# Kernel optimization log

Measured on AMD Instinct MI355X. Metric: run time of the kernel, lower is better.

Reference implementation:

```python
import jax, jax.numpy as jnp
import numpy as np

# FCHL19 representation (Christensen et al., JCP 2020), as implemented by
# QMLightning's pairlist_gpu/egto_gpu/fchl_gpu CUDA kernels, re-expressed as
# dense masked pair/triplet tensors (non-periodic: cell/inv_cell empty).
SPECIES = np.array([1.0, 6.0, 7.0, 8.0], dtype=np.float32)
NSPEC = 4
NRS2 = 24
NRS3 = 20
RCUT = 8.0
ETA2 = 0.32
ETA3 = 2.7
TWO_BODY_DECAY = 1.8
THREE_BODY_DECAY = 0.57
THREE_BODY_WEIGHT = float(np.sqrt(ETA3 / np.pi) * 13.4)  # module pre-scales weight
RS2 = np.linspace(0.0, RCUT, NRS2 + 1)[1:].astype(np.float32)
RS3 = np.linspace(0.0, RCUT, NRS3 + 1)[1:].astype(np.float32)
NPAIR = NSPEC * (NSPEC + 1) // 2  # unordered species pairs -> 10

def _pair_map():
    M = np.zeros((NSPEC, NSPEC, NPAIR), np.float32)
    i = 0
    for p in range(NSPEC):
        for q in range(p, NSPEC):
            M[p, q, i] = 1.0
            M[q, p, i] = 1.0
            i += 1
    return M
PAIR_MAP = _pair_map()

B_MOL, MAX_ATOMS = 64, 28


def setup_inputs() -> dict:
    key = jax.random.key(0)
    k1, k2, k3 = jax.random.split(key, 3)
    X = jax.random.uniform(k1, (B_MOL, MAX_ATOMS, 3), jnp.float32) * 6.0
    atom_counts = jax.random.randint(k2, (B_MOL,), 24, MAX_ATOMS + 1).astype(jnp.int32)
    zidx = jax.random.randint(k3, (B_MOL, MAX_ATOMS), 0, NSPEC)
    valid = jnp.arange(MAX_ATOMS)[None, :] < atom_counts[:, None]
    Z = jnp.where(valid, jnp.asarray(SPECIES)[zidx], 0.0).astype(jnp.float32)
    atomIDs = jnp.arange(B_MOL * MAX_ATOMS, dtype=jnp.int32)
    molIDs = jnp.repeat(jnp.arange(B_MOL, dtype=jnp.int32), MAX_ATOMS)
    return {"X": X, "Z": Z, "atomIDs": atomIDs, "molIDs": molIDs, "atom_counts": atom_counts}


def _fchl(X, Z, atom_counts):
    B, N, _ = X.shape
    valid = jnp.arange(N)[None, :] < atom_counts[:, None]               # [B,N]
    diff = X[:, :, None, :] - X[:, None, :, :]                          # [B,N,N,3]
    d2 = jnp.sum(diff * diff, -1)
    eye = jnp.eye(N, dtype=bool)[None]
    pair_ok = valid[:, :, None] & valid[:, None, :] & (~eye)
    r = jnp.sqrt(jnp.where(pair_ok, d2, 1.0))                           # grad-safe distances
    within = pair_ok & (r < RCUT)
    fc = jnp.where(within, 0.5 * (jnp.cos(jnp.pi * r / RCUT) + 1.0), 0.0)
    oh = (Z[:, :, None] == jnp.asarray(SPECIES)[None, None, :]).astype(X.dtype)  # [B,N,S]

    # --- two-body: log-normal radial expansion, 1/r^decay scaling, cosine cutoff ---
    ln = jnp.log1p(ETA2 / (r * r))                                      # sigma^2
    mu = jnp.log(r) - 0.5 * ln
    rs2 = jnp.asarray(RS2)
    norm = 1.0 / (jnp.sqrt(ln)[..., None] * np.float32(np.sqrt(2.0 * np.pi)) * rs2)
    radial2 = (fc / jnp.power(r, TWO_BODY_DECAY))[..., None] * norm * \
        jnp.exp(-(jnp.log(rs2) - mu[..., None]) ** 2 / (2.0 * ln[..., None]))     # [B,N,N,M]
    rep2 = jnp.einsum('bijm,bjs->bism', radial2, oh).reshape(B, N, NSPEC * NRS2)

    # --- three-body: Axilrod-Teller-weighted radial x Fourier(order 1) angular ---
    rij = r[:, :, :, None]   # [B,i,j,1] -> broadcast over k
    rik = r[:, :, None, :]
    rjk = r[:, None, :, :]
    triu = (jnp.arange(N)[:, None] < jnp.arange(N)[None, :])[None, None]  # j<k
    m3 = within[:, :, :, None] & within[:, :, None, :] & triu
    rjk_s = jnp.where(m3, rjk, 1.0)
    cos_i = jnp.where(m3, (rij**2 + rik**2 - rjk_s**2) / (2.0 * rij * rik), 0.0)
    cos_j = (rij**2 + rjk_s**2 - rik**2) / (2.0 * rij * rjk_s)
    cos_k = (rik**2 + rjk_s**2 - rij**2) / (2.0 * rik * rjk_s)
    atm = (1.0 + 3.0 * cos_i * cos_j * cos_k) / jnp.power(rij * rik * rjk_s, THREE_BODY_DECAY)
    w = jnp.where(m3, THREE_BODY_WEIGHT * atm * fc[:, :, :, None] * fc[:, :, None, :], 0.0)
    c = jnp.clip(cos_i, -1.0, 1.0)
    s = jnp.sqrt(jnp.clip(1.0 - c * c, 1e-12, 1.0))
    ang = jnp.stack([2.0 * c, 2.0 * s], -1) * w[..., None]              # [B,N,N,N,2]
    radial3 = jnp.exp(-ETA3 * (0.5 * (rij + rik)[..., None] - jnp.asarray(RS3)) ** 2)  # [B,N,N,N,L]
    pair_oh = jnp.einsum('bjp,bkq,pqP->bjkP', oh, oh, jnp.asarray(PAIR_MAP))           # [B,N,N,10]
    t = jnp.einsum('bijka,bjkP->bijkaP', ang, pair_oh)
    rep3 = jnp.einsum('bijkaP,bijkl->biPla', t, radial3).reshape(B, N, NPAIR * NRS3 * 2)

    return jnp.concatenate([rep2, rep3], -1)  # [B,N,496]


def reference(X, Z, atomIDs, molIDs, atom_counts):
    # atomIDs/molIDs are CUDA block-assignment bookkeeping; math doesn't use them.
    return _fchl(X, Z, atom_counts)
```

## Files before the change

kernel.cpp:

```cpp
#include <hip/hip_runtime.h>

#define B_MOL 64
#define MAXN 28
#define NSPEC 4
#define NRS2 24
#define NRS3 20
#define NPAIR 10
#define NCOMB 378
#define REP2_LEN (NSPEC * NRS2)
#define REP3_LEN (NPAIR * NRS3 * 2)
#define OUT_LEN (REP2_LEN + REP3_LEN)
#define RCUT 8.0f
#define ETA2 0.32f
#define ETA3 2.7f
#define LOG2E 1.4426950408889634f
#define LN2F 0.6931471805599453f
#define W3 12.4225783348083f

__device__ __forceinline__ float hexp2(float x) { return __builtin_amdgcn_exp2f(x); }
__device__ __forceinline__ float hlog2(float x) { return __builtin_amdgcn_logf(x); }
__device__ __forceinline__ float hrcp(float x)  { return __builtin_amdgcn_rcpf(x); }
__device__ __forceinline__ float hrsq(float x)  { return __builtin_amdgcn_rsqf(x); }
__device__ __forceinline__ float hcos_rev(float t) { return __builtin_amdgcn_cosf(t); }

__device__ __forceinline__ void decode_pair(int idx, int& j, int& k) {
    int jj = (int)((55.0f - sqrtf(3025.0f - 8.0f * (float)idx)) * 0.5f);
    while (27 * (jj + 1) - ((jj + 1) * jj) / 2 <= idx) ++jj;
    while (27 * jj - (jj * (jj - 1)) / 2 > idx) --jj;
    int off = 27 * jj - (jj * (jj - 1)) / 2;
    j = jj;
    k = jj + 1 + (idx - off);
}

__global__ __launch_bounds__(256) void fchl_kernel(
    const float* __restrict__ X,
    const float* __restrict__ Z,
    const int* __restrict__ counts,
    float* __restrict__ out)
{
    const int i = blockIdx.x;
    const int b = blockIdx.y;
    const int tid = threadIdx.x;
    const int cnt = counts[b];

    __shared__ float sx[MAXN], sy[MAXN], szc[MAXN];
    __shared__ int   sspec[MAXN];
    __shared__ int   s_win[MAXN];
    __shared__ float s_r[MAXN], s_fc[MAXN], s_mu[MAXN], s_i2ln[MAXN], s_pref[MAXN];
    __shared__ int   cntP[NPAIR], curP[NPAIR], baseP[NPAIR];
    __shared__ float4 s_pair[NCOMB];

    if (tid < MAXN) {
        sx[tid]  = X[(b * MAXN + tid) * 3 + 0];
        sy[tid]  = X[(b * MAXN + tid) * 3 + 1];
        szc[tid] = X[(b * MAXN + tid) * 3 + 2];
        float z = Z[b * MAXN + tid];
        int s = -1;
        if (z == 1.0f) s = 0;
        else if (z == 6.0f) s = 1;
        else if (z == 7.0f) s = 2;
        else if (z == 8.0f) s = 3;
        sspec[tid] = s;
    }
    if (tid < NPAIR) cntP[tid] = 0;
    __syncthreads();

    const bool valid_i = (i < cnt);

    if (tid < MAXN) {
        const int j = tid;
        float dx = sx[i] - sx[j], dy = sy[i] - sy[j], dz = szc[i] - szc[j];
        float r = sqrtf(dx * dx + dy * dy + dz * dz);
        bool w = valid_i && (j < cnt) && (j != i) && (r < RCUT);
        s_win[j] = w ? 1 : 0;
        if (w) {
            float fc = 0.5f * (hcos_rev(r * (1.0f / 16.0f)) + 1.0f);
            float ln = LN2F * hlog2(1.0f + ETA2 * hrcp(r * r));
            float lr = LN2F * hlog2(r);
            s_r[j] = r;
            s_fc[j] = fc;
            s_mu[j] = lr - 0.5f * ln;
            s_i2ln[j] = LOG2E / (2.0f * ln);
            s_pref[j] = fc * hexp2(-1.8f * hlog2(r)) * hrsq(ln);
        } else {
            s_r[j] = 1.0f; s_fc[j] = 0.0f; s_mu[j] = 0.0f;
            s_i2ln[j] = 1.0f; s_pref[j] = 0.0f;
        }
    }
    __syncthreads();

    for (int idx = tid; idx < NCOMB; idx += 256) {
        int j, k; decode_pair(idx, j, k);
        if (s_win[j] && s_win[k]) {
            int pj = sspec[j], pk = sspec[k];
            int p = min(pj, pk), q = max(pj, pk);
            int P = p * NSPEC - (p * (p - 1)) / 2 + (q - p);
            atomicAdd(&cntP[P], 1);
        }
    }
    __syncthreads();
    if (tid == 0) {
        int acc = 0;
        #pragma unroll
        for (int p = 0; p < NPAIR; ++p) {
            baseP[p] = acc; curP[p] = acc; acc += cntP[p];
        }
    }
    __syncthreads();

    for (int idx = tid; idx < NCOMB; idx += 256) {
        int j, k; decode_pair(idx, j, k);
        if (!(s_win[j] && s_win[k])) continue;

        float rij = s_r[j], rik = s_r[k];
        float dx = sx[j] - sx[k], dy = sy[j] - sy[k], dz = szc[j] - szc[k];
        float rjk = sqrtf(dx * dx + dy * dy + dz * dz);

        float rij2 = rij * rij, rik2 = rik * rik, rjk2 = rjk * rjk;
        float cos_i = (rij2 + rik2 - rjk2) * 0.5f * hrcp(rij * rik);
        float cos_j = (rij2 + rjk2 - rik2) * 0.5f * hrcp(rij * rjk);
        float cos_k = (rik2 + rjk2 - rij2) * 0.5f * hrcp(rik * rjk);

        float atm = (1.0f + 3.0f * cos_i * cos_j * cos_k)
                    * hexp2(-0.57f * hlog2(rij * rik * rjk));
        float w = W3 * atm * s_fc[j] * s_fc[k];

        float c = fminf(fmaxf(cos_i, -1.0f), 1.0f);
        float sn = sqrtf(fminf(fmaxf(1.0f - c * c, 1e-12f), 1.0f));

        int pj = sspec[j], pk = sspec[k];
        int p = min(pj, pk), q = max(pj, pk);
        int P = p * NSPEC - (p * (p - 1)) / 2 + (q - p);

        int slot = atomicAdd(&curP[P], 1);
        s_pair[slot] = make_float4(0.5f * (rij + rik), 2.0f * c * w, 2.0f * sn * w, 0.0f);
    }
    __syncthreads();

    float* orow = out + (size_t)(b * MAXN + i) * OUT_LEN;

    if (tid < NPAIR * NRS3) {
        const int P = tid / NRS3;
        const int l = tid % NRS3;
        const float rs = 0.4f * (float)(l + 1);
        float acc0 = 0.0f, acc1 = 0.0f;
        const int s0 = baseP[P], s1 = s0 + cntP[P];
        for (int s = s0; s < s1; ++s) {
            float4 pd = s_pair[s];
            float dd = pd.x - rs;
            float e = hexp2(-(ETA3 * LOG2E) * dd * dd);
            acc0 += pd.y * e;
            acc1 += pd.z * e;
        }
        orow[REP2_LEN + P * (NRS3 * 2) + l * 2 + 0] = acc0;
        orow[REP2_LEN + P * (NRS3 * 2) + l * 2 + 1] = acc1;
    }

    if (tid >= 160) {
        const int t2 = tid - 160;
        const int sp = t2 / NRS2;
        const int m = t2 % NRS2;
        const float rs2 = (float)(m + 1) * (8.0f / 24.0f);
        const float lrs2 = LN2F * hlog2(rs2);
        const float nrm = 0.3989422804014327f / rs2;
        float acc = 0.0f;
        #pragma unroll
        for (int j = 0; j < MAXN; ++j) {
            if (s_win[j] && sspec[j] == sp) {
                float d = lrs2 - s_mu[j];
                acc += s_pref[j] * hexp2(-d * d * s_i2ln[j]);
            }
        }
        orow[sp * NRS2 + m] = acc * nrm;
    }
}

extern "C" void kernel_launch(void* const* d_in, const int* in_sizes, int n_in,
                              void* d_out, int out_size, void* d_ws, size_t ws_size,
                              hipStream_t stream) {
    const float* X = (const float*)d_in[0];
    const float* Z = (const float*)d_in[1];
    const int* counts = (const int*)d_in[4];
    float* out = (float*)d_out;

    dim3 grid(MAXN, B_MOL);
    dim3 block(256);
    hipLaunchKernelGGL(fchl_kernel, grid, block, 0, stream, X, Z, counts, out);
}
```

Baseline: 20.69 us.

## Restructure FCHL kernel phases to cut barriers and overlap two-body work

Replaces the arithmetic pair decode with a constant-memory lookup table. Merges coordinate loading with the pair-distance stage, which removes one barrier. The thread-0 prefix scan is replaced by per-thread prefix sums over the pair counts, removing another barrier. The two-body radial computation moves onto otherwise idle threads during the counting phase, and pair tags are cached in shared memory so the species pair index is not recomputed. In exchange each thread does some redundant prefix-sum work and adds a constant-memory load.

New measurement: 24.17 us. 1.17x slower.

```diff
diff --git a/kernel.cpp b/kernel.cpp
--- a/kernel.cpp
+++ b/kernel.cpp
@@ -23,14 +23,16 @@
 __device__ __forceinline__ float hrsq(float x)  { return __builtin_amdgcn_rsqf(x); }
 __device__ __forceinline__ float hcos_rev(float t) { return __builtin_amdgcn_cosf(t); }
 
-__device__ __forceinline__ void decode_pair(int idx, int& j, int& k) {
-    int jj = (int)((55.0f - sqrtf(3025.0f - 8.0f * (float)idx)) * 0.5f);
-    while (27 * (jj + 1) - ((jj + 1) * jj) / 2 <= idx) ++jj;
-    while (27 * jj - (jj * (jj - 1)) / 2 > idx) --jj;
-    int off = 27 * jj - (jj * (jj - 1)) / 2;
-    j = jj;
-    k = jj + 1 + (idx - off);
+struct PairTab { unsigned short jk[NCOMB]; };
+static constexpr PairTab make_tab() {
+    PairTab t{};
+    int idx = 0;
+    for (int j = 0; j < MAXN; ++j)
+        for (int k = j + 1; k < MAXN; ++k)
+            t.jk[idx++] = (unsigned short)((j << 8) | k);
+    return t;
 }
+__constant__ PairTab PT = make_tab();
 
 __global__ __launch_bounds__(256) void fchl_kernel(
     const float* __restrict__ X,
@@ -47,31 +49,32 @@
     __shared__ int   sspec[MAXN];
     __shared__ int   s_win[MAXN];
     __shared__ float s_r[MAXN], s_fc[MAXN], s_mu[MAXN], s_i2ln[MAXN], s_pref[MAXN];
-    __shared__ int   cntP[NPAIR], curP[NPAIR], baseP[NPAIR];
+    __shared__ int   cntP[NPAIR], curP[NPAIR];
+    __shared__ signed char s_ptag[NCOMB];
     __shared__ float4 s_pair[NCOMB];
 
+    float* orow = out + (size_t)(b * MAXN + i) * OUT_LEN;
+
     if (tid < MAXN) {
-        sx[tid]  = X[(b * MAXN + tid) * 3 + 0];
-        sy[tid]  = X[(b * MAXN + tid) * 3 + 1];
-        szc[tid] = X[(b * MAXN + tid) * 3 + 2];
-        float z = Z[b * MAXN + tid];
+        const int j = tid;
+        float xj = X[(b * MAXN + j) * 3 + 0];
+        float yj = X[(b * MAXN + j) * 3 + 1];
+        float zj = X[(b * MAXN + j) * 3 + 2];
+        sx[j] = xj; sy[j] = yj; szc[j] = zj;
+        float z = Z[b * MAXN + j];
         int s = -1;
         if (z == 1.0f) s = 0;
         else if (z == 6.0f) s = 1;
         else if (z == 7.0f) s = 2;
         else if (z == 8.0f) s = 3;
-        sspec[tid] = s;
-    }
-    if (tid < NPAIR) cntP[tid] = 0;
-    __syncthreads();
+        sspec[j] = s;
 
-    const bool valid_i = (i < cnt);
-
-    if (tid < MAXN) {
-        const int j = tid;
-        float dx = sx[i] - sx[j], dy = sy[i] - sy[j], dz = szc[i] - szc[j];
+        float xi = X[(b * MAXN + i) * 3 + 0];
+        float yi = X[(b * MAXN + i) * 3 + 1];
+        float zi = X[(b * MAXN + i) * 3 + 2];
+        float dx = xi - xj, dy = yi - yj, dz = zi - zj;
         float r = sqrtf(dx * dx + dy * dy + dz * dz);
-        bool w = valid_i && (j < cnt) && (j != i) && (r < RCUT);
+        bool w = (i < cnt) && (j < cnt) && (j != i) && (r < RCUT);
         s_win[j] = w ? 1 : 0;
         if (w) {
             float fc = 0.5f * (hcos_rev(r * (1.0f / 16.0f)) + 1.0f);
@@ -86,31 +89,50 @@
             s_r[j] = 1.0f; s_fc[j] = 0.0f; s_mu[j] = 0.0f;
             s_i2ln[j] = 1.0f; s_pref[j] = 0.0f;
         }
+    } else if (tid >= 64 && tid < 64 + NPAIR) {
+        cntP[tid - 64] = 0;
+        curP[tid - 64] = 0;
     }
     __syncthreads();
 
-    for (int idx = tid; idx < NCOMB; idx += 256) {
-        int j, k; decode_pair(idx, j, k);
-        if (s_win[j] && s_win[k]) {
-            int pj = sspec[j], pk = sspec[k];
-            int p = min(pj, pk), q = max(pj, pk);
-            int P = p * NSPEC - (p * (p - 1)) / 2 + (q - p);
-            atomicAdd(&cntP[P], 1);
+    if (tid < 192) {
+        for (int idx = tid; idx < NCOMB; idx += 192) {
+            int jk = PT.jk[idx];
+            int j = jk >> 8, k = jk & 255;
+            int tag = -1;
+            if (s_win[j] && s_win[k]) {
+                int pj = sspec[j], pk = sspec[k];
+                int p = min(pj, pk), q = max(pj, pk);
+                tag = p * NSPEC - (p * (p - 1)) / 2 + (q - p);
+                atomicAdd(&cntP[tag], 1);
+            }
+            s_ptag[idx] = (signed char)tag;
         }
-    }
-    __syncthreads();
-    if (tid == 0) {
-        int acc = 0;
-        #pragma unroll
-        for (int p = 0; p < NPAIR; ++p) {
-            baseP[p] = acc; curP[p] = acc; acc += cntP[p];
+    } else {
+        for (int t2 = tid - 192; t2 < REP2_LEN; t2 += 64) {
+            const int sp = t2 / NRS2;
+            const int m = t2 % NRS2;
+            const float rs2 = (float)(m + 1) * (8.0f / 24.0f);
+            const float lrs2 = LN2F * hlog2(rs2);
+            const float nrm = 0.3989422804014327f / rs2;
+            float acc = 0.0f;
+            #pragma unroll
+            for (int j = 0; j < MAXN; ++j) {
+                if (s_win[j] && sspec[j] == sp) {
+                    float d = lrs2 - s_mu[j];
+                    acc += s_pref[j] * hexp2(-d * d * s_i2ln[j]);
+                }
+            }
+            orow[sp * NRS2 + m] = acc * nrm;
         }
     }
     __syncthreads();
 
     for (int idx = tid; idx < NCOMB; idx += 256) {
-        int j, k; decode_pair(idx, j, k);
-        if (!(s_win[j] && s_win[k])) continue;
+        int tag = s_ptag[idx];
+        if (tag < 0) continue;
+        int jk = PT.jk[idx];
+        int j = jk >> 8, k = jk & 255;
 
         float rij = s_r[j], rik = s_r[k];
         float dx = sx[j] - sx[k], dy = sy[j] - sy[k], dz = szc[j] - szc[k];
@@ -128,23 +150,24 @@
         float c = fminf(fmaxf(cos_i, -1.0f), 1.0f);
         float sn = sqrtf(fminf(fmaxf(1.0f - c * c, 1e-12f), 1.0f));
 
-        int pj = sspec[j], pk = sspec[k];
-        int p = min(pj, pk), q = max(pj, pk);
-        int P = p * NSPEC - (p * (p - 1)) / 2 + (q - p);
-
-        int slot = atomicAdd(&curP[P], 1);
+        int bs = 0;
+        #pragma unroll
+        for (int p = 0; p < NPAIR - 1; ++p) bs += (p < tag) ? cntP[p] : 0;
+        int slot = bs + atomicAdd(&curP[tag], 1);
         s_pair[slot] = make_float4(0.5f * (rij + rik), 2.0f * c * w, 2.0f * sn * w, 0.0f);
     }
     __syncthreads();
-
-    float* orow = out + (size_t)(b * MAXN + i) * OUT_LEN;
 
     if (tid < NPAIR * NRS3) {
         const int P = tid / NRS3;
         const int l = tid % NRS3;
         const float rs = 0.4f * (float)(l + 1);
+        int s0 = 0;
+        #pragma unroll
+        for (int p = 0; p < NPAIR - 1; ++p) s0 += (p < P) ? cntP[p] : 0;
+        const int s1 = s0 + cntP[P];
         float acc0 = 0.0f, acc1 = 0.0f;
-        const int s0 = baseP[P], s1 = s0 + cntP[P];
+        #pragma unroll 2
         for (int s = s0; s < s1; ++s) {
             float4 pd = s_pair[s];
             float dd = pd.x - rs;
@@ -154,24 +177,6 @@
         }
         orow[REP2_LEN + P * (NRS3 * 2) + l * 2 + 0] = acc0;
         orow[REP2_LEN + P * (NRS3 * 2) + l * 2 + 1] = acc1;
-    }
-
-    if (tid >= 160) {
-        const int t2 = tid - 160;
-        const int sp = t2 / NRS2;
-        const int m = t2 % NRS2;
-        const float rs2 = (float)(m + 1) * (8.0f / 24.0f);
-        const float lrs2 = LN2F * hlog2(rs2);
-        const float nrm = 0.3989422804014327f / rs2;
-        float acc = 0.0f;
-        #pragma unroll
-        for (int j = 0; j < MAXN; ++j) {
-            if (s_win[j] && sspec[j] == sp) {
-                float d = lrs2 - s_mu[j];
-                acc += s_pref[j] * hexp2(-d * d * s_i2ln[j]);
-            }
-        }
-        orow[sp * NRS2 + m] = acc * nrm;
     }
 }
 
```
